# Kernel tuning notes

Measured on AMD Instinct MI355X. Metric: run time of the kernel, lower is better.

The kernel has to match this reference:

```python
import jax, jax.numpy as jnp
import numpy as np

B, CIN, CGD, CE, G, H, W = 4, 256, 256, 64, 4, 80, 80
N = H * W
EPS = 1e-8


def _build_trees(guide_embed):
    # guide_embed: np [B, CE, N]. Minimum spanning tree on the 4-connected pixel
    # grid with edge cost exp(||e_u - e_v||^2) (exp is monotone -> same MST as
    # squared distance), then BFS order rooted at node 0.
    idx = np.arange(N).reshape(H, W)
    eu = np.concatenate([idx[:, :-1].ravel(), idx[:-1, :].ravel()])
    ev = np.concatenate([idx[:, 1:].ravel(), idx[1:, :].ravel()])
    orders, parents = [], []
    for b in range(B):
        fm = guide_embed[b]
        dist = ((fm[:, eu] - fm[:, ev]) ** 2).sum(0)
        root = np.arange(N)

        def find(x):
            while root[x] != x:
                root[x] = root[root[x]]
                x = root[x]
            return x

        adj = [[] for _ in range(N)]
        cnt = 0
        for e in np.argsort(dist, kind='stable'):
            a, b2 = find(eu[e]), find(ev[e])
            if a != b2:
                root[a] = b2
                adj[eu[e]].append(ev[e])
                adj[ev[e]].append(eu[e])
                cnt += 1
                if cnt == N - 1:
                    break
        order = np.zeros(N, np.int32)   # order[k] = node id at BFS position k
        ppos = np.zeros(N, np.int32)    # ppos[k]  = BFS position of parent of order[k]
        pos = np.zeros(N, np.int32)
        seen = np.zeros(N, bool)
        seen[0] = True
        head, tail = 0, 1
        while head < tail:
            x = order[head]
            for y in adj[x]:
                if not seen[y]:
                    seen[y] = True
                    order[tail] = y
                    pos[y] = tail
                    ppos[tail] = pos[x]
                    tail += 1
            head += 1
        orders.append(order)
        parents.append(ppos)
    return np.stack(orders), np.stack(parents)


def setup_inputs():
    key = jax.random.key(0)
    ks = jax.random.split(key, 7)
    feature = jax.random.normal(ks[0], (B, CIN, H, W), jnp.float32)
    guide = jax.random.normal(ks[1], (B, CGD, H, W), jnp.float32)
    # 1x1 convs == channel matmuls; std=0.01 per module init (conf/beta/gamma
    # are randomized instead of zero so the test is non-trivial)
    W_embed = 0.01 * jax.random.normal(ks[2], (CE, CIN), jnp.float32)
    W_conf = 0.05 * jax.random.normal(ks[3], (G, CIN), jnp.float32)
    W_guide = 0.01 * jax.random.normal(ks[4], (CE, CGD), jnp.float32)
    beta = 0.1 * jax.random.normal(ks[5], (G,), jnp.float32)
    gamma = 0.5 * jax.random.normal(ks[6], (1,), jnp.float32)
    # tree is built under no_grad in the original -> precompute (eval path: MST)
    ge = np.einsum('oc,bcn->bon', np.asarray(W_guide), np.asarray(guide).reshape(B, CGD, N))
    order, parent = _build_trees(ge)
    return {"feature": feature, "guide": guide, "W_embed": W_embed,
            "W_conf": W_conf, "W_guide": W_guide, "beta": beta, "gamma": gamma,
            "order": jnp.asarray(order), "parent": jnp.asarray(parent)}


def _group_edge_dist(x, order, parent):
    # x: [B, CE, N]; per-group squared L2 between each BFS node and its parent
    src = jnp.take_along_axis(x, order[:, None, :], axis=2)
    tgt = jnp.take_along_axis(src, parent[:, None, :], axis=2)
    d = (src - tgt) ** 2
    return d.reshape(B, G, CE // G, N).sum(axis=2)  # [B, G, N]


def _tree_filter(fs, w, parent):
    # fs: [N, G, C] node features in BFS order; w: [N, G] weight of edge to parent
    n = fs.shape[0]

    def up(agg, k):  # leaves -> root: subtree aggregation
        return agg.at[parent[k]].add(w[k][:, None] * agg[k]), None

    agg, _ = jax.lax.scan(up, fs, jnp.arange(n - 1, 0, -1))

    def down(out, k):  # root -> leaves: full-tree aggregation
        wk = w[k][:, None]
        return out.at[k].set(agg[k] + wk * (out[parent[k]] - wk * agg[k])), None

    out, _ = jax.lax.scan(down, agg, jnp.arange(1, n))
    return out


def reference(feature, guide, W_embed, W_conf, W_guide, beta, gamma, order, parent):
    f = feature.reshape(B, CIN, N)
    g = guide.reshape(B, CGD, N)  # adaptive_avg_pool2d to same HxW == identity
    embed = jnp.einsum('oc,bcn->bon', W_embed, f)
    guide_embed = jnp.einsum('oc,bcn->bon', W_guide, g)
    conf = jax.nn.sigmoid(jnp.einsum('gc,bcn->bgn', W_conf, f))  # [B, G, N]

    d_e = _group_edge_dist(embed, order, parent)
    d_g = _group_edge_dist(guide_embed, order, parent)
    # edge weight = exp(-d_embed) * exp(-d_guide) * exp(-beta^2) (self/att term)
    w = jnp.exp(-(d_e + d_g + (beta ** 2)[None, :, None]))  # [B, G, N] by BFS pos

    fg = f.reshape(B, G, CIN // G, N) * conf[:, :, None, :]  # conf-reweighted feat
    x = jnp.concatenate([fg, conf[:, :, None, :]], axis=2)   # filter feat & norm together
    xs = jnp.take_along_axis(x, order[:, None, None, :], axis=3)
    xs = xs.transpose(0, 3, 1, 2)                            # [B, N, G, Cpg+1]
    out = jax.vmap(_tree_filter)(xs, w.transpose(0, 2, 1), parent)
    inv = jnp.argsort(order, axis=1)                         # node -> BFS position
    out = jnp.take_along_axis(out, inv[:, :, None, None], axis=1)
    out = out.transpose(0, 2, 3, 1)                          # [B, G, Cpg+1, N]
    filt, norm = out[:, :, :-1, :], out[:, :, -1:, :]
    res = (filt / (EPS + norm)).reshape(B, CIN, N)
    return (gamma[0] * res + f).reshape(B, CIN, H, W)
```

## Files before the change

### kernel.cpp

```cpp
#include <hip/hip_runtime.h>
#include <math.h>

#define NB    4
#define CINC  256
#define NG    4
#define NPIX  6400
#define NROWS 132
#define CHG   65
#define TEPS  1e-8f
#define TP    128
#define KC    32
#define SCH   5
#define SPITCH 6416
#define SWT   320
#define LSC   512

typedef unsigned short u16;
typedef unsigned int   u32;

__global__ __launch_bounds__(256) void gemm_prep_kernel(
    const float* __restrict__ f, const float* __restrict__ g,
    const float* __restrict__ We, const float* __restrict__ Wc,
    const float* __restrict__ Wg, float* __restrict__ emb,
    const int* __restrict__ order, const int* __restrict__ parent,
    u16* __restrict__ par16, int* __restrict__ ls,
    int* __restrict__ nl, int* __restrict__ inv)
{
  __shared__ __align__(16) char smem[50176];
  __shared__ int smax;
  const int bid = blockIdx.x;
  const int tid = threadIdx.x;

  if (bid < 200) {
    const int b  = bid / 50;
    const int t0 = (bid - b*50) * TP;
    const int i = tid >> 4;
    const int j = tid & 15;

    float (*fT)[TP]   = reinterpret_cast<float(*)[TP]>(smem);
    float (*gT)[TP]   = reinterpret_cast<float(*)[TP]>(smem + 16384);
    float (*wTt)[136] = reinterpret_cast<float(*)[136]>(smem + 32768);

    float acc[8][8];
    #pragma unroll
    for (int r = 0; r < 8; ++r)
      #pragma unroll
      for (int p = 0; p < 8; ++p) acc[r][p] = 0.f;
    float accc[8];
    #pragma unroll
    for (int p = 0; p < 8; ++p) accc[p] = 0.f;

    const float* fb = f + (size_t)b*CINC*NPIX;
    const float* gb = g + (size_t)b*CINC*NPIX;

    for (int kc = 0; kc < CINC; kc += KC) {
      {
        int kk = tid >> 3;
        int p  = (tid & 7) * 16;
        const float4* srcf = reinterpret_cast<const float4*>(fb + (size_t)(kc+kk)*NPIX + t0 + p);
        const float4* srcg = reinterpret_cast<const float4*>(gb + (size_t)(kc+kk)*NPIX + t0 + p);
        float4* df = reinterpret_cast<float4*>(&fT[kk][p]);
        float4* dg = reinterpret_cast<float4*>(&gT[kk][p]);
        #pragma unroll
        for (int q = 0; q < 4; ++q) { df[q] = srcf[q]; dg[q] = srcg[q]; }
      }
      for (int s = tid; s < 528; s += 256) {
        int r = s >> 2, kb0 = (s & 3) * 8;
        const float* wsrc;
        if (r < 64)       wsrc = We + r*CINC + kc + kb0;
        else if (r < 128) wsrc = Wg + (r-64)*CINC + kc + kb0;
        else              wsrc = Wc + (r-128)*CINC + kc + kb0;
        const float4* wv = reinterpret_cast<const float4*>(wsrc);
        float4 v0 = wv[0], v1 = wv[1];
        wTt[kb0+0][r]=v0.x; wTt[kb0+1][r]=v0.y; wTt[kb0+2][r]=v0.z; wTt[kb0+3][r]=v0.w;
        wTt[kb0+4][r]=v1.x; wTt[kb0+5][r]=v1.y; wTt[kb0+6][r]=v1.z; wTt[kb0+7][r]=v1.w;
      }
      __syncthreads();

      const float (*xT)[TP] = (i < 8) ? fT : gT;
      for (int kk = 0; kk < KC; ++kk) {
        float4 x0 = *reinterpret_cast<const float4*>(&xT[kk][4*j]);
        float4 x1 = *reinterpret_cast<const float4*>(&xT[kk][64 + 4*j]);
        float4 w0 = *reinterpret_cast<const float4*>(&wTt[kk][8*i]);
        float4 w1 = *reinterpret_cast<const float4*>(&wTt[kk][8*i + 4]);
#define FMA8(r, wv) \
        acc[r][0] += (wv)*x0.x; acc[r][1] += (wv)*x0.y; acc[r][2] += (wv)*x0.z; acc[r][3] += (wv)*x0.w; \
        acc[r][4] += (wv)*x1.x; acc[r][5] += (wv)*x1.y; acc[r][6] += (wv)*x1.z; acc[r][7] += (wv)*x1.w;
        FMA8(0, w0.x) FMA8(1, w0.y) FMA8(2, w0.z) FMA8(3, w0.w)
        FMA8(4, w1.x) FMA8(5, w1.y) FMA8(6, w1.z) FMA8(7, w1.w)
#undef FMA8
        if (i < 4) {
          float wcf = wTt[kk][128 + i];
          accc[0] += wcf*x0.x; accc[1] += wcf*x0.y; accc[2] += wcf*x0.z; accc[3] += wcf*x0.w;
          accc[4] += wcf*x1.x; accc[5] += wcf*x1.y; accc[6] += wcf*x1.z; accc[7] += wcf*x1.w;
        }
      }
      __syncthreads();
    }

    float* eb = emb + (size_t)b*NPIX*NROWS;
    #pragma unroll
    for (int p = 0; p < 8; ++p) {
      int n = t0 + ((p >> 2) * 64) + 4*j + (p & 3);
      float4 v0 = make_float4(acc[0][p], acc[1][p], acc[2][p], acc[3][p]);
      float4 v1 = make_float4(acc[4][p], acc[5][p], acc[6][p], acc[7][p]);
      float* base = eb + (size_t)n*NROWS + 8*i;
      *reinterpret_cast<float4*>(base)     = v0;
      *reinterpret_cast<float4*>(base + 4) = v1;
      if (i < 4) eb[(size_t)n*NROWS + 128 + i] = 1.f / (1.f + expf(-accc[p]));
    }
  } else {
    const int b = bid - 200;
    const int* par = parent + b*NPIX;
    const int* ord = order + b*NPIX;
    u32* pk = reinterpret_cast<u32*>(smem);

    #pragma unroll
    for (int it = 0; it < NPIX/256; ++it) {
      int k = tid + it*256;
      int p = par[k];
      pk[k] = ((u32)p << 16) | (k == 0 ? 0u : 1u);
      inv[b*NPIX + ord[k]] = k;
      par16[b*NPIX + k] = (u16)p;
    }
    __syncthreads();

    for (int r = 0; r < 13; ++r) {
      u32 nv[NPIX/256];
      int done = 1;
      #pragma unroll
      for (int it = 0; it < NPIX/256; ++it) {
        int k = tid + it*256;
        u32 w = pk[k];
        u32 a = w >> 16;
        done &= (a == 0u);
        u32 pw = pk[a];
        nv[it] = (pw & 0xffff0000u) | ((w + pw) & 0xffffu);
      }
      if (__syncthreads_and(done)) break;
      #pragma unroll
      for (int it = 0; it < NPIX/256; ++it) pk[tid + it*256] = nv[it];
      __syncthreads();
    }

    if (tid == 0) smax = 0;
    __syncthreads();
    int m = 0;
    #pragma unroll
    for (int it = 0; it < NPIX/256; ++it) m = max(m, (int)(pk[tid + it*256] & 0xffffu));
    atomicMax(&smax, m);
    __syncthreads();
    if (tid == 0) {
      nl[b] = smax + 1;
      ls[b*(NPIX+2) + smax + 1] = NPIX;
    }
    #pragma unroll
    for (int it = 0; it < NPIX/256; ++it) {
      int k = tid + it*256;
      int lv = (int)(pk[k] & 0xffffu);
      if (k == 0 || lv != (int)(pk[k-1] & 0xffffu)) ls[b*(NPIX+2) + lv] = k;
    }
  }
}

__global__ __launch_bounds__(256) void wgx_kernel(
    const float* __restrict__ emb, const int* __restrict__ order,
    const int* __restrict__ parent, const float* __restrict__ beta,
    const float* __restrict__ f, u16* __restrict__ wq,
    float* __restrict__ aggT)
{
  const int bid = blockIdx.x;
  const int tid = threadIdx.x;
  __shared__ int   s_ord[128];
  __shared__ float s_cf[128];

  if (bid < 100) {
    int idx = bid*256 + tid;
    int b = idx / NPIX;
    int k = idx - b*NPIX;
    int n  = order[idx];
    int kp = parent[idx];
    int np = order[b*NPIX + kp];
    const float4* e0 = reinterpret_cast<const float4*>(emb + ((size_t)b*NPIX + n )*NROWS);
    const float4* e1 = reinterpret_cast<const float4*>(emb + ((size_t)b*NPIX + np)*NROWS);
    float d[NG] = {0.f, 0.f, 0.f, 0.f};
    #pragma unroll
    for (int q = 0; q < 32; ++q) {
      float4 a = e0[q], c = e1[q];
      int gg = (q & 15) >> 2;
      float t0 = a.x-c.x, t1 = a.y-c.y, t2 = a.z-c.z, t3 = a.w-c.w;
      d[gg] += t0*t0 + t1*t1 + t2*t2 + t3*t3;
    }
    #pragma unroll
    for (int gg = 0; gg < NG; ++gg) {
      float bg = beta[gg];
      float w = expf(-(d[gg] + bg*bg));
      wq[((size_t)(b*NG+gg))*NPIX + k] = (u16)(w*65535.f + 0.5f);
    }
  } else {
    const int r = bid - 100;
    const int pair = r & 15, tile = r >> 4;
    const int b = pair >> 2, g = pair & 3;
    const int k0 = tile * 128;

    if (tid < 128) {
      int n = order[b*NPIX + k0 + tid];
      s_ord[tid] = n;
      s_cf[tid]  = emb[((size_t)b*NPIX + n)*NROWS + 128 + g];
    }
    __syncthreads();

    const float* fb = f + (size_t)b*CINC*NPIX + (size_t)g*64*NPIX;
    float* dst = aggT + (size_t)(b*NG+g)*CHG*NPIX + k0;
    const int c0 = tid >> 7;
    const int j  = tid & 127;
    const int n  = s_ord[j];
    const float cf = s_cf[j];
    #pragma unroll 4
    for (int cc = c0; cc < 64; cc += 2) {
      dst[(size_t)cc*NPIX + j] = fb[(size_t)cc*NPIX + n] * cf;
    }
    if (tid < 128) dst[(size_t)64*NPIX + j] = cf;
  }
}

__global__ __launch_bounds__(SWT, 1) void sweep_kernel(
    float* __restrict__ aggT, const u16* __restrict__ wq,
    const u16* __restrict__ par16, const int* __restrict__ ls,
    const int* __restrict__ nl)
{
  extern __shared__ char smem[];
  float* s_agg = (float*)smem;
  u32*  s_pw   = (u32*)(smem + 128320);
  int*  s_ls   = (int*)(smem + 128320 + 25600);

  const int bid = blockIdx.x;
  const int b = bid / (NG*13);
  const int r = bid - b*(NG*13);
  const int g = r / 13;
  const int ch0 = (r - g*13) * SCH;
  const int tid = threadIdx.x;
  const int ld = tid & 63;
  const int cw = tid >> 6;
  const int bg = b*NG + g;

  {
    const float4* src = reinterpret_cast<const float4*>(aggT + ((size_t)bg*CHG + ch0 + cw)*NPIX);
    float4* dst = reinterpret_cast<float4*>(s_agg + cw*SPITCH);
    for (int i = ld; i < NPIX/4; i += 64) dst[i] = src[i];
  }
  {
    const u32* wsrc = reinterpret_cast<const u32*>(wq + (size_t)bg*NPIX);
    const u32* psrc = reinterpret_cast<const u32*>(par16 + (size_t)b*NPIX);
    uint2* dpw = reinterpret_cast<uint2*>(s_pw);
    for (int i = tid; i < NPIX/2; i += SWT) {
      u32 ww = wsrc[i];
      u32 pp = psrc[i];
      uint2 v;
      v.x = ((ww & 0xffffu) << 16) | (pp & 0xffffu);
      v.y = (ww & 0xffff0000u)     | (pp >> 16);
      dpw[i] = v;
    }
  }
  const int* lsb = ls + b*(NPIX+2);
  const int L = nl[b];
  for (int i = tid; i <= L && i < LSC; i += SWT) s_ls[i] = lsb[i];
  __syncthreads();

  const float qs = 1.0f/65535.0f;
  float* sa = s_agg + cw*SPITCH;
  auto LS = [&](int x) -> int { x = min(x, L); return (x < LSC) ? s_ls[x] : lsb[x]; };

  {
    int lev = L-2;
    int A = LS(lev), Bv = LS(lev+1), Cv = LS(lev+2);
    while (lev >= 0) {
      int nxt = (lev > 0) ? LS(lev-1) : 0;
      for (int k = Bv + ld; k < Cv; k += 64) {
        u32 pw = s_pw[k];
        float wv = (float)(pw >> 16) * qs;
        atomicAdd(&sa[pw & 0xffffu], wv * sa[k]);
      }
      asm volatile("" ::: "memory");
      Cv = Bv; Bv = A; A = nxt; --lev;
    }
  }

  {
    int lev = 1;
    int A = LS(1), Bv = LS(2);
    while (lev < L) {
      int nxt = LS(lev+2);
      for (int k = A + ld; k < Bv; k += 64) {
        u32 pw = s_pw[k];
        float wv = (float)(pw >> 16) * qs;
        float a  = sa[k];
        float op = sa[pw & 0xffffu];
        sa[k] = fmaf(wv, op - wv*a, a);
      }
      asm volatile("" ::: "memory");
      A = Bv; Bv = nxt; ++lev;
    }
  }

  __syncthreads();

  {
    float4* dst = reinterpret_cast<float4*>(aggT + ((size_t)bg*CHG + ch0 + cw)*NPIX);
    const float4* srcp = reinterpret_cast<const float4*>(s_agg + cw*SPITCH);
    for (int i = ld; i < NPIX/4; i += 64) dst[i] = srcp[i];
  }
}

__global__ __launch_bounds__(256) void epilogue_kernel(
    const float* __restrict__ aggT, const int* __restrict__ inv,
    const float* __restrict__ f, const float* __restrict__ gamma,
    float* __restrict__ out)
{
  const int bid = blockIdx.x;
  const int b = bid & 3, tile = bid >> 2;
  const int n0 = tile * 64;
  const int tid = threadIdx.x;
  const int g = tid >> 6, j = tid & 63;

  __shared__ int s_k[64];
  if (tid < 64) s_k[tid] = inv[b*NPIX + n0 + tid];
  __syncthreads();

  const int k = s_k[j];
  const float* at = aggT + (size_t)(b*NG + g)*CHG*NPIX;
  const float rn = 1.f / (TEPS + at[(size_t)64*NPIX + k]);
  const float gam = gamma[0];
  const float* fb = f   + (size_t)b*CINC*NPIX + (size_t)g*64*NPIX;
  float*       ob = out + (size_t)b*CINC*NPIX + (size_t)g*64*NPIX;
  #pragma unroll 4
  for (int cc = 0; cc < 64; ++cc) {
    float val = at[(size_t)cc*NPIX + k];
    float fv  = fb[(size_t)cc*NPIX + n0 + j];
    ob[(size_t)cc*NPIX + n0 + j] = fmaf(gam, val*rn, fv);
  }
}

extern "C" void kernel_launch(void* const* d_in, const int* in_sizes, int n_in,
                              void* d_out, int out_size, void* d_ws, size_t ws_size,
                              hipStream_t stream)
{
  const float* f     = (const float*)d_in[0];
  const float* g     = (const float*)d_in[1];
  const float* We    = (const float*)d_in[2];
  const float* Wc    = (const float*)d_in[3];
  const float* Wg    = (const float*)d_in[4];
  const float* beta  = (const float*)d_in[5];
  const float* gamma = (const float*)d_in[6];
  const int* order   = (const int*)d_in[7];
  const int* parent  = (const int*)d_in[8];
  float* out = (float*)d_out;

  char* ws = (char*)d_ws;
  size_t off = 0;
  auto carve = [&](size_t bytes) -> void* {
    void* p = ws + off;
    off = (off + bytes + 255) & ~(size_t)255;
    return p;
  };
  float* emb = (float*)carve((size_t)NB*NPIX*NROWS*4);
  float* aggT= (float*)carve((size_t)NB*NG*CHG*NPIX*4);
  u16*  wq   = (u16*) carve((size_t)NB*NG*NPIX*2);
  u16*  par16= (u16*) carve((size_t)NB*NPIX*2);
  int*  ls   = (int*) carve((size_t)NB*(NPIX+2)*4);
  int*  nl   = (int*) carve((size_t)NB*4);
  int*  inv  = (int*) carve((size_t)NB*NPIX*4);

  const int sweep_lds = 128320 + 25600 + 2048;
  hipFuncSetAttribute((const void*)sweep_kernel,
                      hipFuncAttributeMaxDynamicSharedMemorySize, sweep_lds);

  hipLaunchKernelGGL(gemm_prep_kernel, dim3(204),          dim3(256), 0, stream,
                     f, g, We, Wc, Wg, emb, order, parent, par16, ls, nl, inv);
  hipLaunchKernelGGL(wgx_kernel,       dim3(900),          dim3(256), 0, stream,
                     emb, order, parent, beta, f, wq, aggT);
  hipLaunchKernelGGL(sweep_kernel,     dim3(NB*NG*13),     dim3(SWT), sweep_lds, stream,
                     aggT, wq, par16, ls, nl);
  hipLaunchKernelGGL(epilogue_kernel,  dim3((NPIX/64)*NB), dim3(256), 0, stream,
                     aggT, inv, f, gamma, out);
}
```

Before: 354.2 us.

## Fuse normalization epilogue into tree sweep kernel, recomputing norm channel per block

```diff
diff --git a/kernel.cpp b/kernel.cpp
--- a/kernel.cpp
+++ b/kernel.cpp
@@ -10,7 +10,7 @@
 #define TEPS  1e-8f
 #define TP    128
 #define KC    32
-#define SCH   5
+#define SCH   4
 #define SPITCH 6416
 #define SWT   320
 #define LSC   512
@@ -225,9 +225,11 @@
 }
 
 __global__ __launch_bounds__(SWT, 1) void sweep_kernel(
-    float* __restrict__ aggT, const u16* __restrict__ wq,
+    const float* __restrict__ aggT, const u16* __restrict__ wq,
     const u16* __restrict__ par16, const int* __restrict__ ls,
-    const int* __restrict__ nl)
+    const int* __restrict__ nl, const int* __restrict__ inv,
+    const float* __restrict__ f, const float* __restrict__ gamma,
+    float* __restrict__ out)
 {
   extern __shared__ char smem[];
   float* s_agg = (float*)smem;
@@ -235,17 +237,18 @@
   int*  s_ls   = (int*)(smem + 128320 + 25600);
 
   const int bid = blockIdx.x;
-  const int b = bid / (NG*13);
-  const int r = bid - b*(NG*13);
-  const int g = r / 13;
-  const int ch0 = (r - g*13) * SCH;
+  const int b = bid / (NG*16);
+  const int r = bid - b*(NG*16);
+  const int g = r / 16;
+  const int ch0 = (r - g*16) * SCH;
   const int tid = threadIdx.x;
   const int ld = tid & 63;
   const int cw = tid >> 6;
   const int bg = b*NG + g;
 
   {
-    const float4* src = reinterpret_cast<const float4*>(aggT + ((size_t)bg*CHG + ch0 + cw)*NPIX);
+    const int pc = (cw < 4) ? (ch0 + cw) : 64;
+    const float4* src = reinterpret_cast<const float4*>(aggT + ((size_t)bg*CHG + pc)*NPIX);
     float4* dst = reinterpret_cast<float4*>(s_agg + cw*SPITCH);
     for (int i = ld; i < NPIX/4; i += 64) dst[i] = src[i];
   }
@@ -306,38 +309,20 @@
   __syncthreads();
 
   {
-    float4* dst = reinterpret_cast<float4*>(aggT + ((size_t)bg*CHG + ch0 + cw)*NPIX);
-    const float4* srcp = reinterpret_cast<const float4*>(s_agg + cw*SPITCH);
-    for (int i = ld; i < NPIX/4; i += 64) dst[i] = srcp[i];
-  }
-}
-
-__global__ __launch_bounds__(256) void epilogue_kernel(
-    const float* __restrict__ aggT, const int* __restrict__ inv,
-    const float* __restrict__ f, const float* __restrict__ gamma,
-    float* __restrict__ out)
-{
-  const int bid = blockIdx.x;
-  const int b = bid & 3, tile = bid >> 2;
-  const int n0 = tile * 64;
-  const int tid = threadIdx.x;
-  const int g = tid >> 6, j = tid & 63;
-
-  __shared__ int s_k[64];
-  if (tid < 64) s_k[tid] = inv[b*NPIX + n0 + tid];
-  __syncthreads();
-
-  const int k = s_k[j];
-  const float* at = aggT + (size_t)(b*NG + g)*CHG*NPIX;
-  const float rn = 1.f / (TEPS + at[(size_t)64*NPIX + k]);
-  const float gam = gamma[0];
-  const float* fb = f   + (size_t)b*CINC*NPIX + (size_t)g*64*NPIX;
-  float*       ob = out + (size_t)b*CINC*NPIX + (size_t)g*64*NPIX;
-  #pragma unroll 4
-  for (int cc = 0; cc < 64; ++cc) {
-    float val = at[(size_t)cc*NPIX + k];
-    float fv  = fb[(size_t)cc*NPIX + n0 + j];
-    ob[(size_t)cc*NPIX + n0 + j] = fmaf(gam, val*rn, fv);
+    const float gam = gamma[0];
+    const int* invb = inv + b*NPIX;
+    const float* fch = f   + (size_t)b*CINC*NPIX + (size_t)(g*64 + ch0)*NPIX;
+    float*       och = out + (size_t)b*CINC*NPIX + (size_t)(g*64 + ch0)*NPIX;
+    const float* s_nrm = s_agg + 4*SPITCH;
+    for (int n = tid; n < NPIX; n += SWT) {
+      int k = invb[n];
+      float rn = 1.f / (TEPS + s_nrm[k]);
+      #pragma unroll
+      for (int c = 0; c < SCH; ++c) {
+        float val = s_agg[c*SPITCH + k];
+        och[(size_t)c*NPIX + n] = fmaf(gam, val*rn, fch[(size_t)c*NPIX + n]);
+      }
+    }
   }
 }
 
@@ -379,8 +364,6 @@
                      f, g, We, Wc, Wg, emb, order, parent, par16, ls, nl, inv);
   hipLaunchKernelGGL(wgx_kernel,       dim3(900),          dim3(256), 0, stream,
                      emb, order, parent, beta, f, wq, aggT);
-  hipLaunchKernelGGL(sweep_kernel,     dim3(NB*NG*13),     dim3(SWT), sweep_lds, stream,
-                     aggT, wq, par16, ls, nl);
-  hipLaunchKernelGGL(epilogue_kernel,  dim3((NPIX/64)*NB), dim3(256), 0, stream,
-                     aggT, inv, f, gamma, out);
+  hipLaunchKernelGGL(sweep_kernel,     dim3(NB*NG*16),     dim3(SWT), sweep_lds, stream,
+                     aggT, wq, par16, ls, nl, inv, f, gamma, out);
 }
```

Measured after the change: 321.5 us. 1.1x faster.
